# Kernel optimization log

Hardware: AMD Instinct MI355X
Metric: run time of the kernel (lower is better)

The kernel has to match this reference:

```python
import jax, jax.numpy as jnp
import numpy as np

N_NODES = 50000
N_EDGES = 800000
IN_DIM = 128
HID = 64
OUT_DIM = 128
N_GRAPHS = 256


def setup_inputs() -> dict:
    key = jax.random.key(0)
    ks = jax.random.split(key, 8)
    x = jax.random.normal(ks[0], (N_NODES, IN_DIM), dtype=jnp.float32)
    edge_index = jax.random.randint(ks[1], (2, N_EDGES), 0, N_NODES, dtype=jnp.int64)
    batch = jnp.sort(jax.random.randint(ks[2], (N_NODES,), 0, N_GRAPHS, dtype=jnp.int64))
    # Glorot-ish init for GCN weights, zero bias (PyG default bias=True)
    W1 = jax.random.normal(ks[3], (IN_DIM, HID), dtype=jnp.float32) / np.sqrt(IN_DIM)
    b1 = jnp.zeros((HID,), dtype=jnp.float32)
    W2 = jax.random.normal(ks[4], (HID, HID), dtype=jnp.float32) / np.sqrt(HID)
    b2 = jnp.zeros((HID,), dtype=jnp.float32)
    W3 = jax.random.normal(ks[5], (HID, OUT_DIM), dtype=jnp.float32) / np.sqrt(HID)
    b3 = jnp.zeros((OUT_DIM,), dtype=jnp.float32)
    return {"x": x, "edge_index": edge_index, "batch": batch, "num_graphs": N_GRAPHS,
            "W1": W1, "b1": b1, "W2": W2, "b2": b2, "W3": W3, "b3": b3}


def _gcn_norm(edge_index, n_nodes):
    # PyG GCNConv default: add self-loops, symmetric D^{-1/2}(A+I)D^{-1/2} norm.
    loops = jnp.arange(n_nodes, dtype=edge_index.dtype)
    src = jnp.concatenate([edge_index[0], loops])  # [E + N]
    dst = jnp.concatenate([edge_index[1], loops])
    deg = jax.ops.segment_sum(jnp.ones_like(dst, dtype=jnp.float32), dst,
                              num_segments=n_nodes)
    dinv = jnp.where(deg > 0, jax.lax.rsqrt(jnp.maximum(deg, 1.0)), 0.0)
    norm = dinv[src] * dinv[dst]  # [E + N]
    return src, dst, norm


def _gcn_conv(x, W, b, src, dst, norm, n_nodes):
    h = x @ W                                  # [N, F_out] dense GEMM
    msg = h[src] * norm[:, None]               # gather + scale  [E+N, F_out]
    agg = jax.ops.segment_sum(msg, dst, num_segments=n_nodes)
    return agg + b


def reference(x, edge_index, batch, num_graphs, W1, b1, W2, b2, W3, b3):
    n_nodes = x.shape[0]
    src, dst, norm = _gcn_norm(edge_index, n_nodes)
    h = jax.nn.gelu(_gcn_conv(x, W1, b1, src, dst, norm, n_nodes))
    h = jax.nn.gelu(_gcn_conv(h, W2, b2, src, dst, norm, n_nodes))
    h = _gcn_conv(h, W3, b3, src, dst, norm, n_nodes)
    # global_mean_pool over batch segment ids
    sums = jax.ops.segment_sum(h, batch, num_segments=num_graphs)
    counts = jax.ops.segment_sum(jnp.ones((n_nodes,), dtype=h.dtype), batch,
                                 num_segments=num_graphs)
    return sums / jnp.maximum(counts, 1.0)[:, None]
```

## Files before the change

### kernel.cpp

```cpp
#include <hip/hip_runtime.h>
#include <hip/hip_fp16.h>
#include <math.h>

#define N_NODES   50000
#define N_EDGES   800000
#define IN_DIM    128
#define HID       64
#define OUT_DIM   128
#define N_GRAPHS  256
#define MAX_DEG   64

typedef _Float16 half8 __attribute__((ext_vector_type(8)));
typedef float floatx4 __attribute__((ext_vector_type(4)));


__global__ void k_build(const int* __restrict__ src, const int* __restrict__ dst,
                        int* __restrict__ deg, int* __restrict__ col) {
    int e = blockIdx.x * blockDim.x + threadIdx.x;
    if (e < N_EDGES) {
        int d = dst[e];
        int pos = atomicAdd(&deg[d], 1);
        if (pos < MAX_DEG) col[d * MAX_DEG + pos] = src[e];
    }
}

__global__ void k_dinv(const int* __restrict__ deg, float* __restrict__ dinv) {
    int n = blockIdx.x * blockDim.x + threadIdx.x;
    if (n < N_NODES) dinv[n] = rsqrtf((float)(deg[n] + 1));
}

__global__ void k_xcvt(const float* __restrict__ x, const float* __restrict__ dinv,
                       __half* __restrict__ xh) {
    int idx = blockIdx.x * blockDim.x + threadIdx.x;
    if (idx < N_NODES * IN_DIM / 4) {
        int row = idx >> 5;
        float dv = dinv[row];
        float4 v = ((const float4*)x)[idx];
        __half2 h0 = __floats2half2_rn(v.x * dv, v.y * dv);
        __half2 h1 = __floats2half2_rn(v.z * dv, v.w * dv);
        ((__half2*)xh)[2 * idx]     = h0;
        ((__half2*)xh)[2 * idx + 1] = h1;
    }
}

__global__ void k_pack(const float* __restrict__ W, __half* __restrict__ Wt, int K) {
    int idx = blockIdx.x * blockDim.x + threadIdx.x;
    int total = (K / 8) * 64;
    if (idx < total) {
        int g = idx >> 6, n = idx & 63;
#pragma unroll
        for (int i = 0; i < 8; i++)
            Wt[idx * 8 + i] = __float2half(W[(8 * g + i) * 64 + n]);
    }
}


template <int K>
__global__ __launch_bounds__(256) void k_mfma(const __half* __restrict__ A,
                                              const __half* __restrict__ Bp,
                                              __half* __restrict__ C) {
    constexpr int S = K / 32;
    int wv   = threadIdx.x >> 6;
    int lane = threadIdx.x & 63;
    int quad = lane >> 4, l15 = lane & 15;
    int row0 = blockIdx.x * 64 + wv * 16;
    if (row0 >= N_NODES) return;

    half8 bf[S][4];
#pragma unroll
    for (int s = 0; s < S; s++)
#pragma unroll
        for (int j = 0; j < 4; j++)
            bf[s][j] = *(const half8*)(Bp + ((size_t)((4 * s + quad) * 64 + 16 * j + l15)) * 8);

    floatx4 acc[4];
#pragma unroll
    for (int j = 0; j < 4; j++) acc[j] = 0.f;

    int arow = row0 + l15;
#pragma unroll
    for (int s = 0; s < S; s++) {
        half8 af = *(const half8*)(A + (size_t)arow * K + 32 * s + quad * 8);
#pragma unroll
        for (int j = 0; j < 4; j++)
            acc[j] = __builtin_amdgcn_mfma_f32_16x16x32_f16(af, bf[s][j], acc[j], 0, 0, 0);
    }
#pragma unroll
    for (int j = 0; j < 4; j++)
#pragma unroll
        for (int r = 0; r < 4; r++) {
            int row = row0 + quad * 4 + r;
            C[(size_t)row * 64 + 16 * j + l15] = __float2half(acc[j][r]);
        }
}


__global__ __launch_bounds__(256) void k_agg(const __half* __restrict__ T,
                                             const int* __restrict__ col,
                                             const int* __restrict__ indeg,
                                             const float* __restrict__ dinv,
                                             const float* __restrict__ b,
                                             __half* __restrict__ OUT, int mode) {
    int lane = threadIdx.x & 63;
    int wv   = threadIdx.x >> 6;
    int q = lane >> 4, t = lane & 15;
    int d = (blockIdx.x * 4 + wv) * 4 + q;
    int dg = indeg[d]; if (dg > MAX_DEG) dg = MAX_DEG;
    int m1 = max(dg, __shfl_xor(dg, 16));
    int mx = max(m1, __shfl_xor(m1, 32));

    uint2 u = *(const uint2*)(T + (size_t)d * HID + 4 * t);
    __half2 ha = *(__half2*)&u.x, hb = *(__half2*)&u.y;
    float4 acc = make_float4(__low2float(ha), __high2float(ha), __low2float(hb), __high2float(hb));

    for (int base = 0; base < mx; base += 16) {
        int c = 0;
        if (base + t < dg) c = col[d * MAX_DEG + base + t];
        int lim = mx - base; if (lim > 16) lim = 16;
        for (int i = 0; i < lim; i++) {
            int s = __shfl(c, q * 16 + i, 64);
            uint2 v = *(const uint2*)(T + (size_t)s * HID + 4 * t);
            if (base + i < dg) {
                __half2 va = *(__half2*)&v.x, vb = *(__half2*)&v.y;
                acc.x += __low2float(va); acc.y += __high2float(va);
                acc.z += __low2float(vb); acc.w += __high2float(vb);
            }
        }
    }

    float dv = dinv[d];
    float o[4] = {acc.x * dv, acc.y * dv, acc.z * dv, acc.w * dv};
    if (mode == 0) {
#pragma unroll
        for (int j = 0; j < 4; j++) {
            float v = o[j] + b[4 * t + j];
            float u2 = 0.7978845608028654f * (v + 0.044715f * v * v * v);
            o[j] = 0.5f * v * (1.0f + tanhf(u2)) * dv;
        }
    }
    __half2 s0 = __floats2half2_rn(o[0], o[1]);
    __half2 s1 = __floats2half2_rn(o[2], o[3]);
    uint2 st; st.x = *(unsigned*)&s0; st.y = *(unsigned*)&s1;
    *(uint2*)(OUT + (size_t)d * HID + 4 * t) = st;
}


__global__ __launch_bounds__(256) void k_pool_out(const __half* __restrict__ A,
                                                  const int* __restrict__ batch,
                                                  const float* __restrict__ W3,
                                                  const float* __restrict__ b3,
                                                  float* __restrict__ out) {
    int g = blockIdx.x;
    int lo = 0, hi = N_NODES;
    while (lo < hi) { int m = (lo + hi) >> 1; if (batch[m] < g) lo = m + 1; else hi = m; }
    int lo2 = lo, hi2 = N_NODES;
    while (lo2 < hi2) { int m = (lo2 + hi2) >> 1; if (batch[m] < g + 1) lo2 = m + 1; else hi2 = m; }
    int start = lo, end = lo2;

    int lane = threadIdx.x & 63;
    int wave = threadIdx.x >> 6;
    float acc = 0.f;
    for (int n = start + wave; n < end; n += 4)
        acc += __half2float(A[(size_t)n * HID + lane]);

    __shared__ float part[4][HID];
    __shared__ float pooled[HID];
    part[wave][lane] = acc;
    __syncthreads();
    if (threadIdx.x < HID)
        pooled[threadIdx.x] = part[0][threadIdx.x] + part[1][threadIdx.x] +
                              part[2][threadIdx.x] + part[3][threadIdx.x];
    __syncthreads();

    if (threadIdx.x < OUT_DIM) {
        float cntf = (float)(end - start);
        float inv = 1.0f / fmaxf(cntf, 1.0f);
        float s = 0.f;
#pragma unroll
        for (int k = 0; k < HID; k++) s += pooled[k] * W3[k * OUT_DIM + threadIdx.x];
        out[g * OUT_DIM + threadIdx.x] = (s + cntf * b3[threadIdx.x]) * inv;
    }
}


extern "C" void kernel_launch(void* const* d_in, const int* in_sizes, int n_in,
                              void* d_out, int out_size, void* d_ws, size_t ws_size,
                              hipStream_t stream) {
    const float* x     = (const float*)d_in[0];
    const int*   ei    = (const int*)d_in[1];
    const int*   batch = (const int*)d_in[2];
    const float* W1    = (const float*)d_in[4];
    const float* b1    = (const float*)d_in[5];
    const float* W2    = (const float*)d_in[6];
    const float* b2    = (const float*)d_in[7];
    const float* W3    = (const float*)d_in[8];
    const float* b3    = (const float*)d_in[9];
    float* out = (float*)d_out;

    const int* esrc = ei;
    const int* edst = ei + N_EDGES;

    int*    deg  = (int*)d_ws;
    float*  dinv = (float*)(deg + N_NODES);
    int*    col  = (int*)(dinv + N_NODES);
    __half* t    = (__half*)(col + (size_t)N_NODES * MAX_DEG);
    __half* p    = t + (size_t)N_NODES * HID;
    __half* xh   = p + (size_t)N_NODES * HID;
    __half* Wt1  = xh + (size_t)N_NODES * IN_DIM;
    __half* Wt2  = Wt1 + IN_DIM * HID;

    hipMemsetAsync(deg, 0, (size_t)N_NODES * 4, stream);

    const int EB = (N_EDGES + 255) / 256;

    k_build<<<EB, 256, 0, stream>>>(esrc, edst, deg, col);
    k_dinv<<<(N_NODES + 255) / 256, 256, 0, stream>>>(deg, dinv);
    k_xcvt<<<(N_NODES * IN_DIM / 4 + 255) / 256, 256, 0, stream>>>(x, dinv, xh);
    k_pack<<<((IN_DIM / 8) * 64 + 255) / 256, 256, 0, stream>>>(W1, Wt1, IN_DIM);
    k_pack<<<((HID / 8) * 64 + 255) / 256, 256, 0, stream>>>(W2, Wt2, HID);

    const int GB = (N_NODES + 63) / 64;
    const int AB = N_NODES / 16;

    k_mfma<IN_DIM><<<GB, 256, 0, stream>>>(xh, Wt1, t);
    k_agg<<<AB, 256, 0, stream>>>(t, col, deg, dinv, b1, p, 0);
    k_mfma<HID><<<GB, 256, 0, stream>>>(p, Wt2, t);
    k_agg<<<AB, 256, 0, stream>>>(t, col, deg, dinv, b2, p, 0);
    k_agg<<<AB, 256, 0, stream>>>(p, col, deg, dinv, b3, t, 1);
    k_pool_out<<<N_GRAPHS, 256, 0, stream>>>(t, batch, W3, b3, out);
}
```

Measured before the change: 254.8 us.

## Partition CSR build by destination, fuse x conversion into GEMM, unroll gather

The edge-bucketing kernel now has each block scan a 4096-edge chunk and handle only destinations in one of 8 node partitions. This keeps the atomics and column writes within a smaller address range, at the cost of reading the dst array 8 times. The separate fp32-to-fp16 scaling pass over x is removed: the first MFMA GEMM now reads fp32 x directly and applies dinv in registers, saving one full write and read of the half-precision copy. The aggregation loop is unrolled by 4 so four neighbour row loads are issued before they are accumulated, raising memory-level parallelism.

```diff
diff --git a/kernel.cpp b/kernel.cpp
--- a/kernel.cpp
+++ b/kernel.cpp
@@ -9,38 +9,37 @@
 #define OUT_DIM   128
 #define N_GRAPHS  256
 #define MAX_DEG   64
+#define PARTS     8
+#define PSIZE     (N_NODES / PARTS)
+#define EPB       4096
 
 typedef _Float16 half8 __attribute__((ext_vector_type(8)));
 typedef float floatx4 __attribute__((ext_vector_type(4)));
 
 
-__global__ void k_build(const int* __restrict__ src, const int* __restrict__ dst,
-                        int* __restrict__ deg, int* __restrict__ col) {
-    int e = blockIdx.x * blockDim.x + threadIdx.x;
-    if (e < N_EDGES) {
-        int d = dst[e];
-        int pos = atomicAdd(&deg[d], 1);
-        if (pos < MAX_DEG) col[d * MAX_DEG + pos] = src[e];
+__global__ __launch_bounds__(256) void k_build(const int* __restrict__ src,
+                                               const int* __restrict__ dst,
+                                               int* __restrict__ deg, int* __restrict__ col) {
+    int p     = blockIdx.x & (PARTS - 1);
+    int chunk = blockIdx.x >> 3;
+    int base  = chunk * EPB;
+    int lo = p * PSIZE, hi = lo + PSIZE;
+#pragma unroll
+    for (int j = 0; j < EPB / 256; j++) {
+        int e = base + j * 256 + threadIdx.x;
+        if (e < N_EDGES) {
+            int d = dst[e];
+            if (d >= lo && d < hi) {
+                int pos = atomicAdd(&deg[d], 1);
+                if (pos < MAX_DEG) col[d * MAX_DEG + pos] = src[e];
+            }
+        }
     }
 }
 
 __global__ void k_dinv(const int* __restrict__ deg, float* __restrict__ dinv) {
     int n = blockIdx.x * blockDim.x + threadIdx.x;
     if (n < N_NODES) dinv[n] = rsqrtf((float)(deg[n] + 1));
-}
-
-__global__ void k_xcvt(const float* __restrict__ x, const float* __restrict__ dinv,
-                       __half* __restrict__ xh) {
-    int idx = blockIdx.x * blockDim.x + threadIdx.x;
-    if (idx < N_NODES * IN_DIM / 4) {
-        int row = idx >> 5;
-        float dv = dinv[row];
-        float4 v = ((const float4*)x)[idx];
-        __half2 h0 = __floats2half2_rn(v.x * dv, v.y * dv);
-        __half2 h1 = __floats2half2_rn(v.z * dv, v.w * dv);
-        ((__half2*)xh)[2 * idx]     = h0;
-        ((__half2*)xh)[2 * idx + 1] = h1;
-    }
 }
 
 __global__ void k_pack(const float* __restrict__ W, __half* __restrict__ Wt, int K) {
@@ -55,11 +54,11 @@
 }
 
 
-template <int K>
-__global__ __launch_bounds__(256) void k_mfma(const __half* __restrict__ A,
-                                              const __half* __restrict__ Bp,
-                                              __half* __restrict__ C) {
-    constexpr int S = K / 32;
+__global__ __launch_bounds__(256) void k_mfma1(const float* __restrict__ A,
+                                               const float* __restrict__ dinv,
+                                               const __half* __restrict__ Bp,
+                                               __half* __restrict__ C) {
+    constexpr int K = IN_DIM, S = K / 32;
     int wv   = threadIdx.x >> 6;
     int lane = threadIdx.x & 63;
     int quad = lane >> 4, l15 = lane & 15;
@@ -78,6 +77,50 @@
     for (int j = 0; j < 4; j++) acc[j] = 0.f;
 
     int arow = row0 + l15;
+    float dv = dinv[arow];
+#pragma unroll
+    for (int s = 0; s < S; s++) {
+        float4 xa = *(const float4*)(A + (size_t)arow * K + 32 * s + quad * 8);
+        float4 xb = *(const float4*)(A + (size_t)arow * K + 32 * s + quad * 8 + 4);
+        half8 af;
+        af[0] = (_Float16)(xa.x * dv); af[1] = (_Float16)(xa.y * dv);
+        af[2] = (_Float16)(xa.z * dv); af[3] = (_Float16)(xa.w * dv);
+        af[4] = (_Float16)(xb.x * dv); af[5] = (_Float16)(xb.y * dv);
+        af[6] = (_Float16)(xb.z * dv); af[7] = (_Float16)(xb.w * dv);
+#pragma unroll
+        for (int j = 0; j < 4; j++)
+            acc[j] = __builtin_amdgcn_mfma_f32_16x16x32_f16(af, bf[s][j], acc[j], 0, 0, 0);
+    }
+#pragma unroll
+    for (int j = 0; j < 4; j++)
+#pragma unroll
+        for (int r = 0; r < 4; r++)
+            C[(size_t)(row0 + quad * 4 + r) * 64 + 16 * j + l15] = __float2half(acc[j][r]);
+}
+
+
+__global__ __launch_bounds__(256) void k_mfma2(const __half* __restrict__ A,
+                                               const __half* __restrict__ Bp,
+                                               __half* __restrict__ C) {
+    constexpr int K = HID, S = K / 32;
+    int wv   = threadIdx.x >> 6;
+    int lane = threadIdx.x & 63;
+    int quad = lane >> 4, l15 = lane & 15;
+    int row0 = blockIdx.x * 64 + wv * 16;
+    if (row0 >= N_NODES) return;
+
+    half8 bf[S][4];
+#pragma unroll
+    for (int s = 0; s < S; s++)
+#pragma unroll
+        for (int j = 0; j < 4; j++)
+            bf[s][j] = *(const half8*)(Bp + ((size_t)((4 * s + quad) * 64 + 16 * j + l15)) * 8);
+
+    floatx4 acc[4];
+#pragma unroll
+    for (int j = 0; j < 4; j++) acc[j] = 0.f;
+
+    int arow = row0 + l15;
 #pragma unroll
     for (int s = 0; s < S; s++) {
         half8 af = *(const half8*)(A + (size_t)arow * K + 32 * s + quad * 8);
@@ -88,12 +131,16 @@
 #pragma unroll
     for (int j = 0; j < 4; j++)
 #pragma unroll
-        for (int r = 0; r < 4; r++) {
-            int row = row0 + quad * 4 + r;
-            C[(size_t)row * 64 + 16 * j + l15] = __float2half(acc[j][r]);
-        }
-}
-
+        for (int r = 0; r < 4; r++)
+            C[(size_t)(row0 + quad * 4 + r) * 64 + 16 * j + l15] = __float2half(acc[j][r]);
+}
+
+
+__device__ __forceinline__ void addv(float4& acc, uint2 v) {
+    __half2 va = *(__half2*)&v.x, vb = *(__half2*)&v.y;
+    acc.x += __low2float(va); acc.y += __high2float(va);
+    acc.z += __low2float(vb); acc.w += __high2float(vb);
+}
 
 __global__ __launch_bounds__(256) void k_agg(const __half* __restrict__ T,
                                              const int* __restrict__ col,
@@ -110,21 +157,31 @@
     int mx = max(m1, __shfl_xor(m1, 32));
 
     uint2 u = *(const uint2*)(T + (size_t)d * HID + 4 * t);
-    __half2 ha = *(__half2*)&u.x, hb = *(__half2*)&u.y;
-    float4 acc = make_float4(__low2float(ha), __high2float(ha), __low2float(hb), __high2float(hb));
+    float4 acc = make_float4(0.f, 0.f, 0.f, 0.f);
+    addv(acc, u);
 
     for (int base = 0; base < mx; base += 16) {
-        int c = 0;
-        if (base + t < dg) c = col[d * MAX_DEG + base + t];
+        int c = (base + t < dg) ? col[d * MAX_DEG + base + t] : 0;
         int lim = mx - base; if (lim > 16) lim = 16;
-        for (int i = 0; i < lim; i++) {
+        int i = 0;
+        for (; i + 4 <= lim; i += 4) {
+            int s0 = __shfl(c, q * 16 + i,     64);
+            int s1 = __shfl(c, q * 16 + i + 1, 64);
+            int s2 = __shfl(c, q * 16 + i + 2, 64);
+            int s3 = __shfl(c, q * 16 + i + 3, 64);
+            uint2 v0 = *(const uint2*)(T + (size_t)s0 * HID + 4 * t);
+            uint2 v1 = *(const uint2*)(T + (size_t)s1 * HID + 4 * t);
+            uint2 v2 = *(const uint2*)(T + (size_t)s2 * HID + 4 * t);
+            uint2 v3 = *(const uint2*)(T + (size_t)s3 * HID + 4 * t);
+            if (base + i     < dg) addv(acc, v0);
+            if (base + i + 1 < dg) addv(acc, v1);
+            if (base + i + 2 < dg) addv(acc, v2);
+            if (base + i + 3 < dg) addv(acc, v3);
+        }
+        for (; i < lim; i++) {
             int s = __shfl(c, q * 16 + i, 64);
             uint2 v = *(const uint2*)(T + (size_t)s * HID + 4 * t);
-            if (base + i < dg) {
-                __half2 va = *(__half2*)&v.x, vb = *(__half2*)&v.y;
-                acc.x += __low2float(va); acc.y += __high2float(va);
-                acc.z += __low2float(vb); acc.w += __high2float(vb);
-            }
+            if (base + i < dg) addv(acc, v);
         }
     }
 
@@ -205,26 +262,23 @@
     int*    col  = (int*)(dinv + N_NODES);
     __half* t    = (__half*)(col + (size_t)N_NODES * MAX_DEG);
     __half* p    = t + (size_t)N_NODES * HID;
-    __half* xh   = p + (size_t)N_NODES * HID;
-    __half* Wt1  = xh + (size_t)N_NODES * IN_DIM;
+    __half* Wt1  = p + (size_t)N_NODES * HID;
     __half* Wt2  = Wt1 + IN_DIM * HID;
 
     hipMemsetAsync(deg, 0, (size_t)N_NODES * 4, stream);
 
-    const int EB = (N_EDGES + 255) / 256;
-
-    k_build<<<EB, 256, 0, stream>>>(esrc, edst, deg, col);
+    const int CHUNKS = (N_EDGES + EPB - 1) / EPB;
+    k_build<<<CHUNKS * PARTS, 256, 0, stream>>>(esrc, edst, deg, col);
     k_dinv<<<(N_NODES + 255) / 256, 256, 0, stream>>>(deg, dinv);
-    k_xcvt<<<(N_NODES * IN_DIM / 4 + 255) / 256, 256, 0, stream>>>(x, dinv, xh);
     k_pack<<<((IN_DIM / 8) * 64 + 255) / 256, 256, 0, stream>>>(W1, Wt1, IN_DIM);
     k_pack<<<((HID / 8) * 64 + 255) / 256, 256, 0, stream>>>(W2, Wt2, HID);
 
     const int GB = (N_NODES + 63) / 64;
     const int AB = N_NODES / 16;
 
-    k_mfma<IN_DIM><<<GB, 256, 0, stream>>>(xh, Wt1, t);
+    k_mfma1<<<GB, 256, 0, stream>>>(x, dinv, Wt1, t);
     k_agg<<<AB, 256, 0, stream>>>(t, col, deg, dinv, b1, p, 0);
-    k_mfma<HID><<<GB, 256, 0, stream>>>(p, Wt2, t);
+    k_mfma2<<<GB, 256, 0, stream>>>(p, Wt2, t);
     k_agg<<<AB, 256, 0, stream>>>(t, col, deg, dinv, b2, p, 0);
     k_agg<<<AB, 256, 0, stream>>>(p, col, deg, dinv, b3, t, 1);
     k_pool_out<<<N_GRAPHS, 256, 0, stream>>>(t, batch, W3, b3, out);
```

Result: faster. 221.1 us (-13.2%).
